# Performance work log

Measured on AMD Instinct MI355X. Metric: run time of the kernel, lower is better.

## Reference

```python
import jax, jax.numpy as jnp
import numpy as np

N, D_IN, D_H, D_OUT, M = 256, 768, 768, 512, 100000


def setup_inputs() -> dict:
    key = jax.random.key(0)
    ks = jax.random.split(key, 8)
    img_feats = jax.random.normal(ks[0], (N, D_IN), dtype=jnp.float32)
    w1 = jax.random.normal(ks[1], (D_H, D_IN), dtype=jnp.float32) * (1.0 / np.sqrt(D_IN))
    b1 = jax.random.normal(ks[2], (D_H,), dtype=jnp.float32) * 0.01
    w2 = jax.random.normal(ks[3], (D_OUT, D_H), dtype=jnp.float32) * (1.0 / np.sqrt(D_H))
    b2 = jax.random.normal(ks[4], (D_OUT,), dtype=jnp.float32) * 0.01
    logit_scale = jnp.asarray(np.log(1.0 / 0.07), dtype=jnp.float32)
    loc = jax.random.normal(ks[5], (M, D_OUT), dtype=jnp.float32)
    loc_feats = loc / jnp.linalg.norm(loc, axis=1, keepdims=True)  # pre-normalized gallery
    gps_gallery = jax.random.uniform(ks[6], (M, 2), dtype=jnp.float32, minval=-90.0, maxval=90.0)
    return {
        "img_feats": img_feats, "w1": w1, "b1": b1, "w2": w2, "b2": b2,
        "logit_scale": logit_scale, "loc_feats": loc_feats,
        "gps_gallery": gps_gallery, "top_k": 5,
    }


def reference(img_feats, w1, b1, w2, b2, logit_scale, loc_feats, gps_gallery, top_k):
    # Tsfm MLP head: Linear -> ReLU -> Linear
    h = jax.nn.relu(img_feats @ w1.T + b1)            # [N, D_H]
    img = h @ w2.T + b2                               # [N, D_OUT]
    # F.normalize(dim=1)
    img_n = img / jnp.linalg.norm(img, axis=1, keepdims=True)
    # forward_cached: scaled cosine-similarity logits against 100K gallery
    logits = jnp.exp(logit_scale) * (img_n @ loc_feats.T)  # [N, M]
    # predict: softmax over full gallery row, then top-k retrieval
    probs = jax.nn.softmax(logits, axis=-1)
    top_vals, top_idx = jax.lax.top_k(probs, top_k)   # [N, k]
    top_pred_gps = gps_gallery[top_idx[0]]            # [k, 2] (first image, as in original)
    top_pred_prob = top_vals[0]                       # [k]
    return (logits, top_pred_gps, top_pred_prob)
```

## Files before the change

### kernel.cpp

```cpp
#include <hip/hip_runtime.h>
#include <math.h>

#define N_IMG 256
#define DIN   768
#define DH    768
#define DOUT  512
#define M_GAL 100000
#define CAP   2048
#define MT    392

typedef __bf16 bf16_t;
typedef __bf16 bf16x8 __attribute__((ext_vector_type(8)));
typedef float  f32x4  __attribute__((ext_vector_type(4)));

#define OFF_H      0
#define OFF_IMG    (N_IMG*DH)
#define OFF_IMGN   (OFF_IMG  + N_IMG*DOUT)
#define OFF_IMGT   (OFF_IMGN + N_IMG*DOUT)
#define OFF_STATS  (OFF_IMGT + N_IMG*DOUT/2)
#define OFF_CIDX   (OFF_STATS + 4)

#define OUT_GPS  ((size_t)N_IMG * (size_t)M_GAL)
#define OUT_PROB (OUT_GPS + 10)

__device__ inline unsigned fkey(float x) {
  unsigned u = __float_as_uint(x);
  return (u & 0x80000000u) ? ~u : (u | 0x80000000u);
}
__device__ inline float fkey_inv(unsigned k) {
  unsigned u = (k & 0x80000000u) ? (k ^ 0x80000000u) : ~k;
  return __uint_as_float(u);
}

template<int KDIM, int NCOLS, bool RELU>
__global__ __launch_bounds__(256) void mlp_gemm(const float* __restrict__ A,
    const float* __restrict__ B, const float* __restrict__ bias,
    float* __restrict__ C, unsigned* stats_init) {
  if (stats_init && blockIdx.x == 0 && blockIdx.y == 0 && threadIdx.x == 0) {
    stats_init[0] = 0u; stats_init[1] = 0u; stats_init[2] = 0u;
  }
  __shared__ float As[32][34];
  __shared__ float Bs[32][34];
  const int t  = threadIdx.x;
  const int rowbase = blockIdx.y * 32;
  const int colbase = blockIdx.x * 32;
  const int sm = t >> 3;
  const int kc = (t & 7) << 2;
  const int ty = t >> 4, tx = t & 15;
  float a00 = 0.f, a01 = 0.f, a10 = 0.f, a11 = 0.f;
  for (int kt = 0; kt < KDIM; kt += 32) {
    float4 av = *(const float4*)(A + (size_t)(rowbase + sm) * KDIM + kt + kc);
    float4 bv = *(const float4*)(B + (size_t)(colbase + sm) * KDIM + kt + kc);
    __syncthreads();
    As[kc+0][sm] = av.x; As[kc+1][sm] = av.y; As[kc+2][sm] = av.z; As[kc+3][sm] = av.w;
    Bs[kc+0][sm] = bv.x; Bs[kc+1][sm] = bv.y; Bs[kc+2][sm] = bv.z; Bs[kc+3][sm] = bv.w;
    __syncthreads();
#pragma unroll
    for (int j = 0; j < 32; ++j) {
      float2 a = *(const float2*)(&As[j][2*ty]);
      float2 b = *(const float2*)(&Bs[j][2*tx]);
      a00 = fmaf(a.x, b.x, a00); a01 = fmaf(a.x, b.y, a01);
      a10 = fmaf(a.y, b.x, a10); a11 = fmaf(a.y, b.y, a11);
    }
  }
  const int r0 = rowbase + 2*ty;
  const int c0 = colbase + 2*tx;
  const float bb0 = bias[c0], bb1 = bias[c0+1];
  float v00 = a00 + bb0, v01 = a01 + bb1, v10 = a10 + bb0, v11 = a11 + bb1;
  if (RELU) {
    v00 = fmaxf(v00, 0.f); v01 = fmaxf(v01, 0.f);
    v10 = fmaxf(v10, 0.f); v11 = fmaxf(v11, 0.f);
  }
  C[(size_t)r0*NCOLS + c0]       = v00; C[(size_t)r0*NCOLS + c0 + 1]     = v01;
  C[(size_t)(r0+1)*NCOLS + c0]   = v10; C[(size_t)(r0+1)*NCOLS + c0 + 1] = v11;
}

__global__ __launch_bounds__(256) void norm_cast_kernel(const float* __restrict__ img,
    float* __restrict__ img_n, bf16_t* __restrict__ img_t) {
  const int row = blockIdx.x, t = threadIdx.x;
  const float v0 = img[row*DOUT + t];
  const float v1 = img[row*DOUT + 256 + t];
  float s = v0*v0 + v1*v1;
  for (int o = 32; o > 0; o >>= 1) s += __shfl_down(s, o);
  __shared__ float ws4[4];
  if ((t & 63) == 0) ws4[t >> 6] = s;
  __syncthreads();
  const float tot = ws4[0] + ws4[1] + ws4[2] + ws4[3];
  const float inv = 1.0f / sqrtf(tot);
  const float n0 = v0 * inv, n1 = v1 * inv;
  img_n[row*DOUT + t]       = n0;
  img_n[row*DOUT + 256 + t] = n1;
  const int k0 = t, k1 = t + 256;
  img_t[(((k0 >> 3)*N_IMG) + row)*8 + (k0 & 7)] = (bf16_t)n0;
  img_t[(((k1 >> 3)*N_IMG) + row)*8 + (k1 & 7)] = (bf16_t)n1;
}

__global__ __launch_bounds__(256) void logits_kernel(const float* __restrict__ loc,
    const bf16_t* __restrict__ img_t, const float* __restrict__ ls,
    float* __restrict__ out, float* __restrict__ sumexp, unsigned* __restrict__ maxkey) {
  __shared__ bf16_t Asl[64 * 64 * 8];
  const int t = threadIdx.x;
  const int w = t >> 6, l = t & 63;
  const int bx = blockIdx.x;
  const int mtile = (bx & 7) + (bx >> 5) * 8;
  const int ntile = (bx >> 3) & 3;
  const int mb = mtile * 256;
  const int nb = ntile * 64;

#pragma unroll
  for (int r = 0; r < 16; ++r) {
    const int c = r * 4 + w;
    __builtin_amdgcn_global_load_lds(
        (__attribute__((address_space(1))) void*)(img_t + ((size_t)c * N_IMG + nb + l) * 8),
        (__attribute__((address_space(3))) void*)(Asl + (c * 64 + l) * 8),
        16, 0, 0);
  }
  __syncthreads();

  const int lr = l & 15, lq = l >> 4;
  const int mw = mb + w * 64;
  f32x4 acc[4][4];
#pragma unroll
  for (int i = 0; i < 4; ++i)
#pragma unroll
    for (int j = 0; j < 4; ++j)
      acc[i][j] = (f32x4){0.f, 0.f, 0.f, 0.f};

  int mrow[4];
#pragma unroll
  for (int j = 0; j < 4; ++j) {
    int m = mw + j * 16 + lr;
    mrow[j] = m < M_GAL ? m : (M_GAL - 1);
  }

#pragma unroll 2
  for (int kt = 0; kt < 16; ++kt) {
    float4 b0[4], b1[4];
#pragma unroll
    for (int j = 0; j < 4; ++j) {
      const float* p = loc + (size_t)mrow[j] * 512 + kt * 32 + lq * 8;
      b0[j] = *(const float4*)p;
      b1[j] = *(const float4*)(p + 4);
    }
    bf16x8 af[4];
#pragma unroll
    for (int i = 0; i < 4; ++i)
      af[i] = *(const bf16x8*)(Asl + ((kt * 4 + lq) * 64 + i * 16 + lr) * 8);
#pragma unroll
    for (int j = 0; j < 4; ++j) {
      bf16x8 bfr;
      bfr[0] = (bf16_t)b0[j].x; bfr[1] = (bf16_t)b0[j].y;
      bfr[2] = (bf16_t)b0[j].z; bfr[3] = (bf16_t)b0[j].w;
      bfr[4] = (bf16_t)b1[j].x; bfr[5] = (bf16_t)b1[j].y;
      bfr[6] = (bf16_t)b1[j].z; bfr[7] = (bf16_t)b1[j].w;
#pragma unroll
      for (int i = 0; i < 4; ++i)
        acc[i][j] = __builtin_amdgcn_mfma_f32_16x16x32_bf16(af[i], bfr, acc[i][j], 0, 0, 0);
    }
  }

  const float scale = expf(ls[0]);
  if (ntile == 0) {
    float mx = -1e30f, se = 0.f;
    if (lq == 0) {
#pragma unroll
      for (int j = 0; j < 4; ++j) {
        const int m = mw + j * 16 + lr;
        if (m < M_GAL) {
          const float v = scale * acc[0][j][0];
          mx = fmaxf(mx, v);
          se += expf(v);
        }
      }
    }
#pragma unroll
    for (int o = 1; o < 64; o <<= 1) {
      mx = fmaxf(mx, __shfl_xor(mx, o));
      se += __shfl_xor(se, o);
    }
    if (l == 0) { atomicAdd(sumexp, se); atomicMax(maxkey, fkey(mx)); }
  }
#pragma unroll
  for (int i = 0; i < 4; ++i) {
    const int imgr = nb + i * 16 + lq * 4;
#pragma unroll
    for (int j = 0; j < 4; ++j) {
      const int gal = mw + j * 16 + lr;
      if (gal < M_GAL) {
        const size_t base = (size_t)imgr * M_GAL + gal;
#pragma unroll
        for (int r = 0; r < 4; ++r)
          out[base + (size_t)r * M_GAL] = scale * acc[i][j][r];
      }
    }
  }
}

__global__ __launch_bounds__(256) void collect_kernel(const float* __restrict__ out,
    const unsigned* __restrict__ maxkey, unsigned* __restrict__ counter,
    int* __restrict__ cidx) {
  const int i = blockIdx.x * 256 + threadIdx.x;
  if (i >= M_GAL) return;
  const float thresh = fkey_inv(*maxkey) - 0.8f;
  if (out[i] > thresh) {
    const unsigned p = atomicAdd(counter, 1u);
    if (p < CAP) cidx[p] = i;
  }
}

__global__ __launch_bounds__(256) void final_kernel(const float* __restrict__ loc,
    const float* __restrict__ img_n, const float* __restrict__ ls,
    const unsigned* __restrict__ counter, const int* __restrict__ cidx,
    const float* __restrict__ gps, const float* __restrict__ sumexp,
    float* __restrict__ out) {
  __shared__ float v[CAP];
  __shared__ int   id[CAP];
  __shared__ float rv[256];
  __shared__ int   ri[256];
  __shared__ int   rs[256];
  __shared__ float a0[DOUT];
  const int t = threadIdx.x;
  const unsigned cnt = *counter;
  const int n = (int)(cnt < CAP ? cnt : CAP);
  const float scale = expf(ls[0]);
  a0[t] = img_n[t]; a0[t + 256] = img_n[t + 256];
  __syncthreads();
  for (int c = t; c < CAP; c += 256) {
    if (c < n) {
      const int gi = cidx[c];
      const float* B = loc + (size_t)gi * 512;
      float s = 0.f;
#pragma unroll 8
      for (int k = 0; k < 512; k += 4) {
        const float4 b = *(const float4*)(B + k);
        s = fmaf(a0[k], b.x, s); s = fmaf(a0[k+1], b.y, s);
        s = fmaf(a0[k+2], b.z, s); s = fmaf(a0[k+3], b.w, s);
      }
      v[c] = scale * s; id[c] = gi;
    } else { v[c] = -1e30f; id[c] = 0x7fffffff; }
  }
  const float se = *sumexp;
  __syncthreads();
  for (int k = 0; k < 5; ++k) {
    float bv = -1e30f; int bidx = 0x7fffffff; int bslot = -1;
    for (int i = t; i < CAP; i += 256) {
      const float vi = v[i]; const int ii = id[i];
      if (vi > bv || (vi == bv && ii < bidx)) { bv = vi; bidx = ii; bslot = i; }
    }
    rv[t] = bv; ri[t] = bidx; rs[t] = bslot;
    __syncthreads();
    for (int s = 128; s > 0; s >>= 1) {
      if (t < s) {
        if (rv[t+s] > rv[t] || (rv[t+s] == rv[t] && ri[t+s] < ri[t])) {
          rv[t] = rv[t+s]; ri[t] = ri[t+s]; rs[t] = rs[t+s];
        }
      }
      __syncthreads();
    }
    if (t == 0) {
      const int sl = rs[0]; const int gi = ri[0]; const float lv = rv[0];
      float g0 = 0.f, g1 = 0.f, pr = 0.f;
      if (sl >= 0 && gi != 0x7fffffff) {
        g0 = gps[(size_t)gi*2]; g1 = gps[(size_t)gi*2 + 1];
        pr = expf(lv) / se;
        v[sl] = -1e30f; id[sl] = 0x7fffffff;
      }
      out[OUT_GPS + 2*k]     = g0;
      out[OUT_GPS + 2*k + 1] = g1;
      out[OUT_PROB + k]      = pr;
    }
    __syncthreads();
  }
}

extern "C" void kernel_launch(void* const* d_in, const int* in_sizes, int n_in,
                              void* d_out, int out_size, void* d_ws, size_t ws_size,
                              hipStream_t stream) {
  const float* img_feats = (const float*)d_in[0];
  const float* w1  = (const float*)d_in[1];
  const float* b1  = (const float*)d_in[2];
  const float* w2  = (const float*)d_in[3];
  const float* b2  = (const float*)d_in[4];
  const float* ls  = (const float*)d_in[5];
  const float* loc = (const float*)d_in[6];
  const float* gps = (const float*)d_in[7];
  float* out = (float*)d_out;
  float* ws  = (float*)d_ws;

  float*    h       = ws + OFF_H;
  float*    img     = ws + OFF_IMG;
  float*    img_n   = ws + OFF_IMGN;
  bf16_t*   img_t   = (bf16_t*)(ws + OFF_IMGT);
  float*    sumexp  = ws + OFF_STATS;
  unsigned* maxkey  = (unsigned*)(ws + OFF_STATS + 1);
  unsigned* counter = (unsigned*)(ws + OFF_STATS + 2);
  int*      cidx    = (int*)(ws + OFF_CIDX);

  mlp_gemm<DIN, DH, true><<<dim3(DH/32, N_IMG/32), 256, 0, stream>>>(
      img_feats, w1, b1, h, (unsigned*)(ws + OFF_STATS));
  mlp_gemm<DH, DOUT, false><<<dim3(DOUT/32, N_IMG/32), 256, 0, stream>>>(
      h, w2, b2, img, nullptr);
  norm_cast_kernel<<<N_IMG, 256, 0, stream>>>(img, img_n, img_t);
  logits_kernel<<<MT * 4, 256, 0, stream>>>(loc, img_t, ls, out, sumexp, maxkey);
  collect_kernel<<<(M_GAL + 255) / 256, 256, 0, stream>>>(out, maxkey, counter, cidx);
  final_kernel<<<1, 256, 0, stream>>>(loc, img_n, ls, counter, cidx, gps, sumexp, out);
}
```

Before: 481.3 us.

## Halve logits tile, software-pipeline gallery loads, and parallelize candidate rescoring

The logits GEMM tile shrinks from 256 to 128 gallery rows per block, doubling the grid, with a 4-blocks-per-SM launch bound and a half-size LDS buffer for the image tile that is loaded in two K halves. Gallery loads are software-pipelined through a three-stage register ring so global reads for step k+2 are issued while step k computes. The single-block final kernel's exact fp32 rescoring of candidates moves into a separate 128-block kernel that computes one dot product per wave, leaving only the top-k selection in the single-block kernel. This targets memory latency in the main GEMM and the serial tail. In exchange it adds an extra barrier and reload mid-GEMM and one more kernel launch.

```diff
diff --git a/kernel.cpp b/kernel.cpp
--- a/kernel.cpp
+++ b/kernel.cpp
@@ -7,7 +7,7 @@
 #define DOUT  512
 #define M_GAL 100000
 #define CAP   2048
-#define MT    392
+#define MT    784
 
 typedef __bf16 bf16_t;
 typedef __bf16 bf16x8 __attribute__((ext_vector_type(8)));
@@ -19,6 +19,7 @@
 #define OFF_IMGT   (OFF_IMGN + N_IMG*DOUT)
 #define OFF_STATS  (OFF_IMGT + N_IMG*DOUT/2)
 #define OFF_CIDX   (OFF_STATS + 4)
+#define OFF_CVAL   (OFF_CIDX + CAP)
 
 #define OUT_GPS  ((size_t)N_IMG * (size_t)M_GAL)
 #define OUT_PROB (OUT_GPS + 10)
@@ -95,20 +96,68 @@
   img_t[(((k1 >> 3)*N_IMG) + row)*8 + (k1 & 7)] = (bf16_t)n1;
 }
 
-__global__ __launch_bounds__(256) void logits_kernel(const float* __restrict__ loc,
+__global__ __launch_bounds__(256, 4) void logits_kernel(const float* __restrict__ loc,
     const bf16_t* __restrict__ img_t, const float* __restrict__ ls,
     float* __restrict__ out, float* __restrict__ sumexp, unsigned* __restrict__ maxkey) {
-  __shared__ bf16_t Asl[64 * 64 * 8];
+  __shared__ bf16_t Asl[32 * 64 * 8];
   const int t = threadIdx.x;
   const int w = t >> 6, l = t & 63;
   const int bx = blockIdx.x;
   const int mtile = (bx & 7) + (bx >> 5) * 8;
   const int ntile = (bx >> 3) & 3;
-  const int mb = mtile * 256;
+  const int mb = mtile * 128;
   const int nb = ntile * 64;
-
-#pragma unroll
-  for (int r = 0; r < 16; ++r) {
+  const int lr = l & 15, lq = l >> 4;
+  const int mw = mb + w * 32;
+
+  const float* bp[2];
+#pragma unroll
+  for (int j = 0; j < 2; ++j) {
+    int m = mw + j * 16 + lr;
+    m = m < M_GAL ? m : (M_GAL - 1);
+    bp[j] = loc + (size_t)m * 512 + lq * 8;
+  }
+
+  f32x4 acc[4][2];
+#pragma unroll
+  for (int i = 0; i < 4; ++i)
+#pragma unroll
+    for (int j = 0; j < 2; ++j)
+      acc[i][j] = (f32x4){0.f, 0.f, 0.f, 0.f};
+
+  float4 B0[3][2], B1[3][2];
+
+#define ISSUE(kt) {                                                  \
+    const int s_ = (kt) % 3;                                         \
+    _Pragma("unroll")                                                \
+    for (int j_ = 0; j_ < 2; ++j_) {                                 \
+      const float* p_ = bp[j_] + (kt) * 32;                          \
+      B0[s_][j_] = *(const float4*)p_;                               \
+      B1[s_][j_] = *(const float4*)(p_ + 4);                         \
+    } }
+
+#define COMPUTE(kt) {                                                \
+    const int kb_ = ((kt) & 7) * 4 + lq;                             \
+    const int s_  = (kt) % 3;                                        \
+    bf16x8 af_[4];                                                   \
+    _Pragma("unroll")                                                \
+    for (int i_ = 0; i_ < 4; ++i_)                                   \
+      af_[i_] = *(const bf16x8*)(Asl + (kb_ * 64 + i_ * 16 + lr) * 8); \
+    _Pragma("unroll")                                                \
+    for (int j_ = 0; j_ < 2; ++j_) {                                 \
+      bf16x8 bf_;                                                    \
+      bf_[0] = (bf16_t)B0[s_][j_].x; bf_[1] = (bf16_t)B0[s_][j_].y;  \
+      bf_[2] = (bf16_t)B0[s_][j_].z; bf_[3] = (bf16_t)B0[s_][j_].w;  \
+      bf_[4] = (bf16_t)B1[s_][j_].x; bf_[5] = (bf16_t)B1[s_][j_].y;  \
+      bf_[6] = (bf16_t)B1[s_][j_].z; bf_[7] = (bf16_t)B1[s_][j_].w;  \
+      _Pragma("unroll")                                              \
+      for (int i_ = 0; i_ < 4; ++i_)                                 \
+        acc[i_][j_] = __builtin_amdgcn_mfma_f32_16x16x32_bf16(af_[i_], bf_, acc[i_][j_], 0, 0, 0); \
+    } }
+
+  ISSUE(0); ISSUE(1);
+#pragma unroll
+  for (int r = 0; r < 8; ++r) {
     const int c = r * 4 + w;
     __builtin_amdgcn_global_load_lds(
         (__attribute__((address_space(1))) void*)(img_t + ((size_t)c * N_IMG + nb + l) * 8),
@@ -117,54 +166,37 @@
   }
   __syncthreads();
 
-  const int lr = l & 15, lq = l >> 4;
-  const int mw = mb + w * 64;
-  f32x4 acc[4][4];
-#pragma unroll
-  for (int i = 0; i < 4; ++i)
-#pragma unroll
-    for (int j = 0; j < 4; ++j)
-      acc[i][j] = (f32x4){0.f, 0.f, 0.f, 0.f};
-
-  int mrow[4];
-#pragma unroll
-  for (int j = 0; j < 4; ++j) {
-    int m = mw + j * 16 + lr;
-    mrow[j] = m < M_GAL ? m : (M_GAL - 1);
-  }
-
-#pragma unroll 2
-  for (int kt = 0; kt < 16; ++kt) {
-    float4 b0[4], b1[4];
-#pragma unroll
-    for (int j = 0; j < 4; ++j) {
-      const float* p = loc + (size_t)mrow[j] * 512 + kt * 32 + lq * 8;
-      b0[j] = *(const float4*)p;
-      b1[j] = *(const float4*)(p + 4);
-    }
-    bf16x8 af[4];
-#pragma unroll
-    for (int i = 0; i < 4; ++i)
-      af[i] = *(const bf16x8*)(Asl + ((kt * 4 + lq) * 64 + i * 16 + lr) * 8);
-#pragma unroll
-    for (int j = 0; j < 4; ++j) {
-      bf16x8 bfr;
-      bfr[0] = (bf16_t)b0[j].x; bfr[1] = (bf16_t)b0[j].y;
-      bfr[2] = (bf16_t)b0[j].z; bfr[3] = (bf16_t)b0[j].w;
-      bfr[4] = (bf16_t)b1[j].x; bfr[5] = (bf16_t)b1[j].y;
-      bfr[6] = (bf16_t)b1[j].z; bfr[7] = (bf16_t)b1[j].w;
-#pragma unroll
-      for (int i = 0; i < 4; ++i)
-        acc[i][j] = __builtin_amdgcn_mfma_f32_16x16x32_bf16(af[i], bfr, acc[i][j], 0, 0, 0);
-    }
-  }
+#pragma unroll
+  for (int kt = 0; kt < 8; ++kt) {
+    ISSUE(kt + 2);
+    COMPUTE(kt);
+  }
+
+  __syncthreads();
+#pragma unroll
+  for (int r = 0; r < 8; ++r) {
+    const int c = r * 4 + w;
+    __builtin_amdgcn_global_load_lds(
+        (__attribute__((address_space(1))) void*)(img_t + ((size_t)(32 + c) * N_IMG + nb + l) * 8),
+        (__attribute__((address_space(3))) void*)(Asl + (c * 64 + l) * 8),
+        16, 0, 0);
+  }
+  __syncthreads();
+
+#pragma unroll
+  for (int kt = 8; kt < 16; ++kt) {
+    if (kt < 14) { ISSUE(kt + 2); }
+    COMPUTE(kt);
+  }
+#undef ISSUE
+#undef COMPUTE
 
   const float scale = expf(ls[0]);
   if (ntile == 0) {
     float mx = -1e30f, se = 0.f;
     if (lq == 0) {
 #pragma unroll
-      for (int j = 0; j < 4; ++j) {
+      for (int j = 0; j < 2; ++j) {
         const int m = mw + j * 16 + lr;
         if (m < M_GAL) {
           const float v = scale * acc[0][j][0];
@@ -184,7 +216,7 @@
   for (int i = 0; i < 4; ++i) {
     const int imgr = nb + i * 16 + lq * 4;
 #pragma unroll
-    for (int j = 0; j < 4; ++j) {
+    for (int j = 0; j < 2; ++j) {
       const int gal = mw + j * 16 + lr;
       if (gal < M_GAL) {
         const size_t base = (size_t)imgr * M_GAL + gal;
@@ -208,9 +240,27 @@
   }
 }
 
-__global__ __launch_bounds__(256) void final_kernel(const float* __restrict__ loc,
+__global__ __launch_bounds__(256) void recompute_kernel(const float* __restrict__ loc,
     const float* __restrict__ img_n, const float* __restrict__ ls,
     const unsigned* __restrict__ counter, const int* __restrict__ cidx,
+    float* __restrict__ cval) {
+  const int w = threadIdx.x >> 6, l = threadIdx.x & 63;
+  const unsigned cnt = *counter;
+  const int n = (int)(cnt < CAP ? cnt : CAP);
+  const float scale = expf(ls[0]);
+  for (int c = blockIdx.x * 4 + w; c < n; c += gridDim.x * 4) {
+    const int idx = cidx[c];
+    const float* B = loc + (size_t)idx * 512;
+    float s = 0.f;
+#pragma unroll
+    for (int e = 0; e < 8; ++e) s = fmaf(img_n[l + e*64], B[l + e*64], s);
+    for (int o = 32; o > 0; o >>= 1) s += __shfl_down(s, o);
+    if (l == 0) cval[c] = scale * s;
+  }
+}
+
+__global__ __launch_bounds__(256) void finalize_kernel(const unsigned* __restrict__ counter,
+    const int* __restrict__ cidx, const float* __restrict__ cval,
     const float* __restrict__ gps, const float* __restrict__ sumexp,
     float* __restrict__ out) {
   __shared__ float v[CAP];
@@ -218,26 +268,12 @@
   __shared__ float rv[256];
   __shared__ int   ri[256];
   __shared__ int   rs[256];
-  __shared__ float a0[DOUT];
   const int t = threadIdx.x;
   const unsigned cnt = *counter;
   const int n = (int)(cnt < CAP ? cnt : CAP);
-  const float scale = expf(ls[0]);
-  a0[t] = img_n[t]; a0[t + 256] = img_n[t + 256];
-  __syncthreads();
-  for (int c = t; c < CAP; c += 256) {
-    if (c < n) {
-      const int gi = cidx[c];
-      const float* B = loc + (size_t)gi * 512;
-      float s = 0.f;
-#pragma unroll 8
-      for (int k = 0; k < 512; k += 4) {
-        const float4 b = *(const float4*)(B + k);
-        s = fmaf(a0[k], b.x, s); s = fmaf(a0[k+1], b.y, s);
-        s = fmaf(a0[k+2], b.z, s); s = fmaf(a0[k+3], b.w, s);
-      }
-      v[c] = scale * s; id[c] = gi;
-    } else { v[c] = -1e30f; id[c] = 0x7fffffff; }
+  for (int i = t; i < CAP; i += 256) {
+    v[i]  = (i < n) ? cval[i] : -1e30f;
+    id[i] = (i < n) ? cidx[i] : 0x7fffffff;
   }
   const float se = *sumexp;
   __syncthreads();
@@ -295,6 +331,7 @@
   unsigned* maxkey  = (unsigned*)(ws + OFF_STATS + 1);
   unsigned* counter = (unsigned*)(ws + OFF_STATS + 2);
   int*      cidx    = (int*)(ws + OFF_CIDX);
+  float*    cval    = ws + OFF_CVAL;
 
   mlp_gemm<DIN, DH, true><<<dim3(DH/32, N_IMG/32), 256, 0, stream>>>(
       img_feats, w1, b1, h, (unsigned*)(ws + OFF_STATS));
@@ -303,5 +340,6 @@
   norm_cast_kernel<<<N_IMG, 256, 0, stream>>>(img, img_n, img_t);
   logits_kernel<<<MT * 4, 256, 0, stream>>>(loc, img_t, ls, out, sumexp, maxkey);
   collect_kernel<<<(M_GAL + 255) / 256, 256, 0, stream>>>(out, maxkey, counter, cidx);
-  final_kernel<<<1, 256, 0, stream>>>(loc, img_n, ls, counter, cidx, gps, sumexp, out);
-}
+  recompute_kernel<<<128, 256, 0, stream>>>(loc, img_n, ls, counter, cidx, cval);
+  finalize_kernel<<<1, 256, 0, stream>>>(counter, cidx, cval, gps, sumexp, out);
+}
```

New measurement: 474.6 us. About the same (-1.4%).
